# Kernel tuning notes

Measured on AMD Instinct MI355X. Metric: run time of the kernel, lower is better.

## Reference

```python
import jax, jax.numpy as jnp
import numpy as np

B, L, D = 4, 2048, 512
H, DK, DV = 8, 64, 64


def setup_inputs() -> dict:
    key = jax.random.key(0)
    ks = jax.random.split(key, 12)
    s = 0.02
    return {
        "query": jax.random.normal(ks[0], (B, L, D), jnp.float32),
        "key": jax.random.normal(ks[1], (B, L, D), jnp.float32),
        "value": jax.random.normal(ks[2], (B, L, D), jnp.float32),
        "attention_mask": jax.random.normal(ks[3], (1, 1, L, L), jnp.float32),
        "Wq": jax.random.normal(ks[4], (D, H * DK), jnp.float32) * s,
        "bq": jnp.zeros((H * DK,), jnp.float32),
        "Wk": jax.random.normal(ks[5], (D, H * DK), jnp.float32) * s,
        "bk": jnp.zeros((H * DK,), jnp.float32),
        "Wv": jax.random.normal(ks[6], (D, H * DV), jnp.float32) * s,
        "bv": jnp.zeros((H * DV,), jnp.float32),
        "Wo": jax.random.normal(ks[7], (H * DV, D), jnp.float32) * s,
        "bo": jnp.zeros((D,), jnp.float32),
    }


def reference(query, key, value, attention_mask, Wq, bq, Wk, bk, Wv, bv, Wo, bo):
    sz_b, len_q, _ = query.shape
    len_k = key.shape[1]
    # projections -> [B, L, H, d]
    q = (query @ Wq + bq).reshape(sz_b, len_q, H, DK)
    k = (key @ Wk + bk).reshape(sz_b, len_k, H, DK)
    v = (value @ Wv + bv).reshape(sz_b, len_k, H, DV)
    # permute(2,0,1,3): heads first -> [H, B, L, d]
    q = jnp.transpose(q, (2, 0, 1, 3))
    k = jnp.transpose(k, (2, 0, 1, 3))
    v = jnp.transpose(v, (2, 0, 1, 3))
    scale = 1.0 / jnp.sqrt(jnp.asarray(DK, q.dtype))
    scores = jnp.einsum('hbqd,hbkd->hbqk', q, k) * scale + attention_mask
    attn = jax.nn.softmax(scores, axis=-1)
    x = jnp.einsum('hbqk,hbkd->hbqd', attn, v)  # [H, B, Lq, Dv]
    # faithful to torch: transpose(1,2) -> [H, Lq, B, Dv] then view(B, Lq, H*Dv)
    x = jnp.transpose(x, (0, 2, 1, 3)).reshape(sz_b, len_q, H * DV)
    return x @ Wo + bo
```

## Files before the change

kernel.cpp:

```cpp
#include <hip/hip_runtime.h>

#define SEQ    2048
#define DMODEL 512
#define NHEAD  8
#define HDIM   64
#define BATCH  4
#define NROWS  65536
#define KSPLIT 2

#define LOG2E  1.4426950408889634f
#define QSCALE 0.18033688011112042f

typedef float f32x4  __attribute__((ext_vector_type(4)));
typedef float f32x16 __attribute__((ext_vector_type(16)));
typedef _Float16 h16x8 __attribute__((ext_vector_type(8)));
typedef _Float16 h16x2 __attribute__((ext_vector_type(2)));
typedef unsigned int u32x2 __attribute__((ext_vector_type(2)));

union U4H { uint4 u; h16x8 h; };
union U1H2 { unsigned int u; h16x2 h; };

static __device__ inline h16x2 pkrtz(float a, float b) {
    return __builtin_bit_cast(h16x2, __builtin_amdgcn_cvt_pkrtz(a, b));
}
static __device__ inline unsigned short f2h(float x) {
    _Float16 h = (_Float16)x;
    return __builtin_bit_cast(unsigned short, h);
}
static __device__ inline void async_cp16(const void* g, void* l) {
    __builtin_amdgcn_global_load_lds(
        (const __attribute__((address_space(1))) unsigned int*)g,
        (__attribute__((address_space(3))) unsigned int*)l,
        16, 0, 0);
}

struct PrepArgs {
    const float *Wq, *Wk, *Wv, *Wo;
    unsigned short *WqT, *WkT, *WvT, *WoT;
    const float *mask; unsigned short *mp;
    const float *aq, *ak, *av;
    unsigned short *dq, *dk, *dv;
};

__global__ __launch_bounds__(256) void prepass(PrepArgs a) {
    const int bid = blockIdx.x;
    const int t = threadIdx.x;

    if (bid < 1024) {
        const int z = bid >> 8, y = (bid >> 4) & 15, x = bid & 15;
        const float* S; unsigned short* D;
        switch (z) {
            case 0: S = a.Wq; D = a.WqT; break;
            case 1: S = a.Wk; D = a.WkT; break;
            case 2: S = a.Wv; D = a.WvT; break;
            default: S = a.Wo; D = a.WoT; break;
        }
        __shared__ float T[32][33];
        const int r = t >> 3, c = (t & 7) * 4;
        const int k0 = x * 32, n0 = y * 32;
        float4 v = *(const float4*)&S[(size_t)(k0 + r) * DMODEL + n0 + c];
        T[r][c] = v.x; T[r][c + 1] = v.y; T[r][c + 2] = v.z; T[r][c + 3] = v.w;
        __syncthreads();
        ushort4 o;
        o.x = f2h(T[c + 0][r]); o.y = f2h(T[c + 1][r]);
        o.z = f2h(T[c + 2][r]); o.w = f2h(T[c + 3][r]);
        *(ushort4*)&D[(size_t)(n0 + r) * DMODEL + k0 + c] = o;
    } else if (bid < 1024 + 4096) {
        int i = (bid - 1024) * 256 + t;
        int k = (i * 4) & (SEQ - 1);
        int q = (i * 4) >> 11;
        float4 v = ((const float4*)a.mask)[i];
        int kt = k >> 6, kl = k & 63;
        int mt = kl >> 5, g = (kl >> 3) & 3, hl = (kl >> 2) & 1;
        size_t base = ((size_t)kt * SEQ + q) * 64 + hl * 32 + mt * 16 + g * 4;
        ushort4 o;
        o.x = f2h(__builtin_amdgcn_exp2f(v.x * LOG2E));
        o.y = f2h(__builtin_amdgcn_exp2f(v.y * LOG2E));
        o.z = f2h(__builtin_amdgcn_exp2f(v.z * LOG2E));
        o.w = f2h(__builtin_amdgcn_exp2f(v.w * LOG2E));
        *(ushort4*)&a.mp[base] = o;
    } else {
        int u = bid - 5120;
        int z = u >> 11, blk = u & 2047;
        const float* S; unsigned short* D;
        switch (z) {
            case 0: S = a.aq; D = a.dq; break;
            case 1: S = a.ak; D = a.dk; break;
            default: S = a.av; D = a.dv; break;
        }
        size_t i = ((size_t)blk * 256 + t) * 8;
        float4 x = *(const float4*)&S[i];
        float4 y = *(const float4*)&S[i + 4];
        U1H2 p0, p1, p2, p3;
        p0.h = pkrtz(x.x, x.y); p1.h = pkrtz(x.z, x.w);
        p2.h = pkrtz(y.x, y.y); p3.h = pkrtz(y.z, y.w);
        *(uint4*)&D[i] = make_uint4(p0.u, p1.u, p2.u, p3.u);
    }
}

template <int EPI>
static __device__ inline void gemm_core16(
    const unsigned short* __restrict__ Ab, const unsigned short* __restrict__ Bt,
    const float* __restrict__ bias, void* __restrict__ Cout, float oscale,
    int bm, int bn)
{
    __shared__ __align__(16) unsigned short As[2][128 * 32];
    __shared__ __align__(16) unsigned short Bs[2][128 * 32];

    const int t = threadIdx.x;
    const int lane = t & 63, w = t >> 6;
    const int wm = w >> 1, wn = w & 1;
    const int c = lane & 15, quad = lane >> 4;
    const int srow = lane >> 2;
    const int sck  = (lane & 3) ^ ((lane >> 3) & 3);

    f32x4 acc[4][4] = {};

    #pragma unroll
    for (int i = 0; i < 2; i++) {
        int row = 32 * w + 16 * i + srow;
        async_cp16(Ab + (size_t)(bm + row) * DMODEL + sck * 8,
                   &As[0][(32 * w + 16 * i) * 32]);
        async_cp16(Bt + (size_t)(bn + row) * DMODEL + sck * 8,
                   &Bs[0][(32 * w + 16 * i) * 32]);
    }
    __syncthreads();

    const int slot8 = (quad ^ ((c >> 1) & 3)) * 8;

    for (int k0 = 0; k0 < DMODEL; k0 += 32) {
        const int cur = (k0 >> 5) & 1;
        if (k0 + 32 < DMODEL) {
            #pragma unroll
            for (int i = 0; i < 2; i++) {
                int row = 32 * w + 16 * i + srow;
                async_cp16(Ab + (size_t)(bm + row) * DMODEL + k0 + 32 + sck * 8,
                           &As[cur ^ 1][(32 * w + 16 * i) * 32]);
                async_cp16(Bt + (size_t)(bn + row) * DMODEL + k0 + 32 + sck * 8,
                           &Bs[cur ^ 1][(32 * w + 16 * i) * 32]);
            }
        }
        U4H af[4], bf[4];
        #pragma unroll
        for (int mt = 0; mt < 4; mt++)
            af[mt].u = *(const uint4*)&As[cur][(wm * 64 + mt * 16 + c) * 32 + slot8];
        #pragma unroll
        for (int nt = 0; nt < 4; nt++)
            bf[nt].u = *(const uint4*)&Bs[cur][(wn * 64 + nt * 16 + c) * 32 + slot8];
        #pragma unroll
        for (int mt = 0; mt < 4; mt++)
            #pragma unroll
            for (int nt = 0; nt < 4; nt++)
                acc[mt][nt] = __builtin_amdgcn_mfma_f32_16x16x32_f16(
                    af[mt].h, bf[nt].h, acc[mt][nt], 0, 0, 0);
        __syncthreads();
    }

    if (EPI == 2) {
        #pragma unroll
        for (int nt = 0; nt < 4; nt++) {
            int ng = bn + wn * 64 + nt * 16 + c;
            int h = ng >> 6, dv = ng & 63;
            float bv = bias[ng];
            #pragma unroll
            for (int mt = 0; mt < 4; mt++) {
                int mg0 = bm + wm * 64 + mt * 16 + quad * 4;
                int bb = mg0 >> 11, key0 = mg0 & (SEQ - 1);
                U1H2 lo, hi;
                lo.h = pkrtz(acc[mt][nt][0] + bv, acc[mt][nt][1] + bv);
                hi.h = pkrtz(acc[mt][nt][2] + bv, acc[mt][nt][3] + bv);
                *(uint2*)&((unsigned short*)Cout)[
                    ((size_t)(bb * NHEAD + h) * HDIM + dv) * SEQ + key0] =
                    make_uint2(lo.u, hi.u);
            }
        }
        return;
    }
    #pragma unroll
    for (int nt = 0; nt < 4; nt++) {
        int ng = bn + wn * 64 + nt * 16 + c;
        float bv = bias[ng];
        #pragma unroll
        for (int mt = 0; mt < 4; mt++) {
            #pragma unroll
            for (int r = 0; r < 4; r++) {
                int mg = bm + wm * 64 + mt * 16 + quad * 4 + r;
                float v = (acc[mt][nt][r] + bv) * oscale;
                if (EPI == 1)
                    ((unsigned short*)Cout)[(size_t)mg * DMODEL + ng] = f2h(v);
                else
                    ((float*)Cout)[(size_t)mg * DMODEL + ng] = v;
            }
        }
    }
}

struct QKVArgs {
    const unsigned short *A0, *A1, *A2;
    const unsigned short *W0, *W1, *W2;
    const float *b0, *b1, *b2;
    unsigned short *o0, *o1, *o2;
};

__global__ __launch_bounds__(256) void gemm_qkv(QKVArgs a) {
    if (blockIdx.z == 2)
        gemm_core16<2>(a.A2, a.W2, a.b2, a.o2, 1.0f, blockIdx.y * 128, blockIdx.x * 128);
    else if (blockIdx.z == 1)
        gemm_core16<1>(a.A1, a.W1, a.b1, a.o1, 1.0f, blockIdx.y * 128, blockIdx.x * 128);
    else
        gemm_core16<1>(a.A0, a.W0, a.b0, a.o0, QSCALE, blockIdx.y * 128, blockIdx.x * 128);
}

__global__ __launch_bounds__(256) void gemm_fin(
    const unsigned short* __restrict__ A, const unsigned short* __restrict__ W,
    const float* __restrict__ bias, float* __restrict__ C) {
    gemm_core16<0>(A, W, bias, C, 1.0f, blockIdx.y * 128, blockIdx.x * 128);
}

__global__ __launch_bounds__(256, 3) void attn5(
    const unsigned short* __restrict__ qb, const unsigned short* __restrict__ kb,
    const unsigned short* __restrict__ vT, const unsigned short* __restrict__ emp,
    unsigned short* __restrict__ Xp, float* __restrict__ Lp)
{
    __shared__ __align__(16) unsigned short Ks[2][64 * 64];
    __shared__ __align__(16) unsigned short Vs[2][64 * 64];

    const int t = threadIdx.x;
    const int lane = t & 63, w = t >> 6;
    const int c32 = lane & 31, hl = lane >> 5;

    const int bid = blockIdx.x;
    const int xcd = bid & 7, slot = bid >> 3;
    const int bh = slot & 31;
    const int comb = (slot >> 5) * 8 + xcd;
    const int split = comb >> 4;
    const int q0 = (comb & 15) * 128;
    const int b = bh >> 3, head = bh & 7;
    const int qg = q0 + w * 32 + c32;

    const unsigned short* qrow = qb + ((size_t)b * SEQ + qg) * DMODEL + head * HDIM;
    U4H Qf[4];
    #pragma unroll
    for (int s = 0; s < 4; s++)
        Qf[s].u = *(const uint4*)&qrow[s * 16 + hl * 8];

    const unsigned short* kgb = kb + (size_t)b * SEQ * DMODEL + head * HDIM
                              + (size_t)split * 1024 * DMODEL;
    const unsigned short* vgb = vT + (size_t)bh * HDIM * SEQ + split * 1024;

    const int srow = lane >> 3;
    const int sch  = (lane & 7) ^ srow;

    {
        #pragma unroll
        for (int i = 0; i < 2; i++) {
            int row = w * 16 + i * 8 + srow;
            async_cp16(&kgb[(size_t)row * DMODEL + sch * 8], &Ks[0][(w * 16 + i * 8) * 64]);
            async_cp16(&vgb[(size_t)row * SEQ + sch * 8],    &Vs[0][(w * 16 + i * 8) * 64]);
        }
    }

    U4H e0, e1, e2, e3;
    {
        const unsigned short* mrow = emp + ((size_t)(split * 16) * SEQ + qg) * 64 + hl * 32;
        e0.u = *(const uint4*)&mrow[0];
        e1.u = *(const uint4*)&mrow[8];
        e2.u = *(const uint4*)&mrow[16];
        e3.u = *(const uint4*)&mrow[24];
    }

    f32x16 O0 = {}, O1 = {};
    float lsum = 0.f;
    const h16x2 one2 = {(_Float16)1.0f, (_Float16)1.0f};

    for (int kt = 0; kt < 1024 / 64; kt++) {
        const int p = kt & 1;
        __syncthreads();

        if (kt + 1 < 1024 / 64) {
            int k0n = (kt + 1) * 64;
            #pragma unroll
            for (int i = 0; i < 2; i++) {
                int row = w * 16 + i * 8 + srow;
                async_cp16(&kgb[(size_t)(k0n + row) * DMODEL + sch * 8],
                           &Ks[p ^ 1][(w * 16 + i * 8) * 64]);
                async_cp16(&vgb[(size_t)row * SEQ + k0n + sch * 8],
                           &Vs[p ^ 1][(w * 16 + i * 8) * 64]);
            }
        }

        U4H f0, f1, f2, f3;
        {
            int ktn = (kt + 1 < 1024 / 64) ? kt + 1 : kt;
            const unsigned short* mrow =
                emp + ((size_t)(split * 16 + ktn) * SEQ + qg) * 64 + hl * 32;
            f0.u = *(const uint4*)&mrow[0];
            f1.u = *(const uint4*)&mrow[8];
            f2.u = *(const uint4*)&mrow[16];
            f3.u = *(const uint4*)&mrow[24];
        }

        const unsigned short* Kp = Ks[p];
        const unsigned short* Vp = Vs[p];

        f32x16 S0 = {}, S1 = {};
        __builtin_amdgcn_s_setprio(1);
        #pragma unroll
        for (int s = 0; s < 4; s++) {
            int fc = 2 * s + hl;
            int sl = (fc ^ (c32 & 7)) * 8;
            U4H ka0, ka1;
            ka0.u = *(const uint4*)&Kp[c32 * 64 + sl];
            ka1.u = *(const uint4*)&Kp[(32 + c32) * 64 + sl];
            S0 = __builtin_amdgcn_mfma_f32_32x32x16_f16(ka0.h, Qf[s].h, S0, 0, 0, 0);
            S1 = __builtin_amdgcn_mfma_f32_32x32x16_f16(ka1.h, Qf[s].h, S1, 0, 0, 0);
        }
        __builtin_amdgcn_s_setprio(0);

        unsigned int Pf[4][4];
        #pragma unroll
        for (int mt = 0; mt < 2; mt++) {
            f32x16 S = mt ? S1 : S0;
            h16x8 ea = (mt ? e2 : e0).h;
            h16x8 eb = (mt ? e3 : e1).h;
            unsigned int u[4][2];
            #pragma unroll
            for (int jj = 0; jj < 8; jj++) {
                _Float16 exl = (jj < 4) ? ea[2 * jj]     : eb[2 * jj - 8];
                _Float16 exh = (jj < 4) ? ea[2 * jj + 1] : eb[2 * jj - 7];
                h16x2 ex = {exl, exh};
                h16x2 pk = pkrtz(__builtin_amdgcn_exp2f(S[2 * jj]),
                                 __builtin_amdgcn_exp2f(S[2 * jj + 1]));
                h16x2 pp = pk * ex;
#if __has_builtin(__builtin_amdgcn_fdot2)
                lsum = __builtin_amdgcn_fdot2(pp, one2, lsum, false);
#else
                lsum += (float)pp[0] + (float)pp[1];
#endif
                u[jj >> 1][jj & 1] = __builtin_bit_cast(unsigned int, pp);
            }
#if __has_builtin(__builtin_amdgcn_permlane32_swap)
            u32x2 rA0 = __builtin_amdgcn_permlane32_swap(u[0][0], u[1][0], false, false);
            u32x2 rA1 = __builtin_amdgcn_permlane32_swap(u[0][1], u[1][1], false, false);
            u32x2 rB0 = __builtin_amdgcn_permlane32_swap(u[2][0], u[3][0], false, false);
            u32x2 rB1 = __builtin_amdgcn_permlane32_swap(u[2][1], u[3][1], false, false);
            Pf[2 * mt + 0][0] = rA0[0]; Pf[2 * mt + 0][1] = rA1[0];
            Pf[2 * mt + 0][2] = rA0[1]; Pf[2 * mt + 0][3] = rA1[1];
            Pf[2 * mt + 1][0] = rB0[0]; Pf[2 * mt + 1][1] = rB1[0];
            Pf[2 * mt + 1][2] = rB0[1]; Pf[2 * mt + 1][3] = rB1[1];
#else
            unsigned int sA0 = hl ? u[0][0] : u[1][0];
            unsigned int sA1 = hl ? u[0][1] : u[1][1];
            unsigned int sB0 = hl ? u[2][0] : u[3][0];
            unsigned int sB1 = hl ? u[2][1] : u[3][1];
            unsigned int rA0 = (unsigned)__shfl_xor((int)sA0, 32, 64);
            unsigned int rA1 = (unsigned)__shfl_xor((int)sA1, 32, 64);
            unsigned int rB0 = (unsigned)__shfl_xor((int)sB0, 32, 64);
            unsigned int rB1 = (unsigned)__shfl_xor((int)sB1, 32, 64);
            Pf[2 * mt + 0][0] = hl ? rA0 : u[0][0];
            Pf[2 * mt + 0][1] = hl ? rA1 : u[0][1];
            Pf[2 * mt + 0][2] = hl ? u[1][0] : rA0;
            Pf[2 * mt + 0][3] = hl ? u[1][1] : rA1;
            Pf[2 * mt + 1][0] = hl ? rB0 : u[2][0];
            Pf[2 * mt + 1][1] = hl ? rB1 : u[2][1];
            Pf[2 * mt + 1][2] = hl ? u[3][0] : rB0;
            Pf[2 * mt + 1][3] = hl ? u[3][1] : rB1;
#endif
        }

        __builtin_amdgcn_s_setprio(1);
        #pragma unroll
        for (int s = 0; s < 4; s++) {
            int kc = 2 * s + hl;
            int sl = (kc ^ (c32 & 7)) * 8;
            U4H va0, va1, pu;
            va0.u = *(const uint4*)&Vp[c32 * 64 + sl];
            va1.u = *(const uint4*)&Vp[(32 + c32) * 64 + sl];
            pu.u = make_uint4(Pf[s][0], Pf[s][1], Pf[s][2], Pf[s][3]);
            O0 = __builtin_amdgcn_mfma_f32_32x32x16_f16(va0.h, pu.h, O0, 0, 0, 0);
            O1 = __builtin_amdgcn_mfma_f32_32x32x16_f16(va1.h, pu.h, O1, 0, 0, 0);
        }
        __builtin_amdgcn_s_setprio(0);

        e0 = f0; e1 = f1; e2 = f2; e3 = f3;
    }

    lsum += __shfl_xor(lsum, 32, 64);
    const size_t j = ((size_t)head * SEQ + qg) * BATCH + b;
    unsigned short* xr = Xp + ((size_t)split * NROWS + j) * HDIM;
    #pragma unroll
    for (int mt = 0; mt < 2; mt++) {
        f32x16 Ov = mt ? O1 : O0;
        #pragma unroll
        for (int g = 0; g < 4; g++) {
            U1H2 lo, hi;
            lo.h = pkrtz(Ov[g * 4 + 0], Ov[g * 4 + 1]);
            hi.h = pkrtz(Ov[g * 4 + 2], Ov[g * 4 + 3]);
            uint2 st = make_uint2(lo.u, hi.u);
            *(uint2*)&xr[mt * 32 + 8 * g + 4 * hl] = st;
        }
    }
    if (hl == 0) Lp[split * NROWS + j] = lsum;
}

__global__ __launch_bounds__(256) void combine_attn(
    const unsigned short* __restrict__ Xp, const float* __restrict__ Lp,
    unsigned short* __restrict__ xb)
{
    int i = blockIdx.x * 256 + threadIdx.x;
    int j = i >> 3, dc = (i & 7) * 8;
    U4H a, b;
    a.u = *(const uint4*)&Xp[(size_t)j * HDIM + dc];
    b.u = *(const uint4*)&Xp[((size_t)NROWS + j) * HDIM + dc];
    float inv = 1.0f / (Lp[j] + Lp[NROWS + j]);
    U4H o;
    #pragma unroll
    for (int p = 0; p < 4; p++) {
        float s0 = ((float)a.h[2 * p]     + (float)b.h[2 * p])     * inv;
        float s1 = ((float)a.h[2 * p + 1] + (float)b.h[2 * p + 1]) * inv;
        h16x2 pk = pkrtz(s0, s1);
        o.h[2 * p] = pk[0]; o.h[2 * p + 1] = pk[1];
    }
    *(uint4*)&xb[(size_t)j * HDIM + dc] = o.u;
}

extern "C" void kernel_launch(void* const* d_in, const int* in_sizes, int n_in,
                              void* d_out, int out_size, void* d_ws, size_t ws_size,
                              hipStream_t stream) {
    const float* query = (const float*)d_in[0];
    const float* key_  = (const float*)d_in[1];
    const float* value = (const float*)d_in[2];
    const float* mask  = (const float*)d_in[3];
    const float* Wq = (const float*)d_in[4];
    const float* bq = (const float*)d_in[5];
    const float* Wk = (const float*)d_in[6];
    const float* bk = (const float*)d_in[7];
    const float* Wv = (const float*)d_in[8];
    const float* bv = (const float*)d_in[9];
    const float* Wo = (const float*)d_in[10];
    const float* bo = (const float*)d_in[11];
    float* out = (float*)d_out;

    const size_t NP = (size_t)BATCH * SEQ * DMODEL;
    unsigned short* ws   = (unsigned short*)d_ws;
    unsigned short* qb16 = ws;
    unsigned short* kb16 = qb16 + NP;
    unsigned short* vT16 = kb16 + NP;
    unsigned short* xb16 = vT16 + NP;
    unsigned short* em16 = xb16 + NP;
    unsigned short* Xp16 = em16 + (size_t)SEQ * SEQ;
    unsigned short* WqT  = Xp16 + (size_t)KSPLIT * NROWS * HDIM;
    unsigned short* WkT  = WqT + DMODEL * DMODEL;
    unsigned short* WvT  = WkT + DMODEL * DMODEL;
    unsigned short* WoT  = WvT + DMODEL * DMODEL;
    float* Lp = (float*)(WoT + DMODEL * DMODEL);

    unsigned short* q16 = xb16;
    unsigned short* k16 = Xp16;
    unsigned short* v16 = Xp16 + NP;

    PrepArgs pa;
    pa.Wq = Wq; pa.Wk = Wk; pa.Wv = Wv; pa.Wo = Wo;
    pa.WqT = WqT; pa.WkT = WkT; pa.WvT = WvT; pa.WoT = WoT;
    pa.mask = mask; pa.mp = em16;
    pa.aq = query; pa.ak = key_; pa.av = value;
    pa.dq = q16; pa.dk = k16; pa.dv = v16;
    prepass<<<dim3(1024 + 4096 + 6144), 256, 0, stream>>>(pa);

    QKVArgs qa;
    qa.A0 = q16;  qa.A1 = k16;  qa.A2 = v16;
    qa.W0 = WqT;  qa.W1 = WkT;  qa.W2 = WvT;
    qa.b0 = bq;   qa.b1 = bk;   qa.b2 = bv;
    qa.o0 = qb16; qa.o1 = kb16; qa.o2 = vT16;
    gemm_qkv<<<dim3(DMODEL / 128, BATCH * SEQ / 128, 3), 256, 0, stream>>>(qa);

    attn5<<<dim3(BATCH * NHEAD * (SEQ / 128) * KSPLIT), 256, 0, stream>>>(
        qb16, kb16, vT16, em16, Xp16, Lp);

    combine_attn<<<dim3(NROWS * 8 / 256), 256, 0, stream>>>(Xp16, Lp, xb16);

    gemm_fin<<<dim3(DMODEL / 128, BATCH * SEQ / 128), 256, 0, stream>>>(
        xb16, WoT, bo, out);
}
```

Baseline: 235.8 us.

## Triple-buffer LDS tiles with vmcnt waits in GEMM and attention kernels

Both the projection GEMM core and the attention kernel now keep three LDS stages instead of two, prefetching two tiles ahead. The full __syncthreads is replaced by explicit s_waitcnt vmcnt plus s_barrier, so each wave waits only for the older async loads. The attention grid is also changed from a 1D XCD-swizzled index to a plain 3D grid, which drops the XCD-locality mapping. The extra LDS may reduce occupancy, and the vmcnt counts must stay exactly in step with the in-flight global loads, including the mask loads.

```diff
diff --git a/kernel.cpp b/kernel.cpp
--- a/kernel.cpp
+++ b/kernel.cpp
@@ -19,6 +19,8 @@
 
 union U4H { uint4 u; h16x8 h; };
 union U1H2 { unsigned int u; h16x2 h; };
+
+#define WAITV(N) asm volatile("s_waitcnt vmcnt(" #N ")" ::: "memory")
 
 static __device__ inline h16x2 pkrtz(float a, float b) {
     return __builtin_bit_cast(h16x2, __builtin_amdgcn_cvt_pkrtz(a, b));
@@ -104,8 +106,8 @@
     const float* __restrict__ bias, void* __restrict__ Cout, float oscale,
     int bm, int bn)
 {
-    __shared__ __align__(16) unsigned short As[2][128 * 32];
-    __shared__ __align__(16) unsigned short Bs[2][128 * 32];
+    __shared__ __align__(16) unsigned short As[3][128 * 32];
+    __shared__ __align__(16) unsigned short Bs[3][128 * 32];
 
     const int t = threadIdx.x;
     const int lane = t & 63, w = t >> 6;
@@ -116,28 +118,36 @@
 
     f32x4 acc[4][4] = {};
 
+    const int NT = DMODEL / 32;
+
     #pragma unroll
-    for (int i = 0; i < 2; i++) {
-        int row = 32 * w + 16 * i + srow;
-        async_cp16(Ab + (size_t)(bm + row) * DMODEL + sck * 8,
-                   &As[0][(32 * w + 16 * i) * 32]);
-        async_cp16(Bt + (size_t)(bn + row) * DMODEL + sck * 8,
-                   &Bs[0][(32 * w + 16 * i) * 32]);
-    }
-    __syncthreads();
+    for (int b2 = 0; b2 < 2; b2++) {
+        #pragma unroll
+        for (int i = 0; i < 2; i++) {
+            int row = 32 * w + 16 * i + srow;
+            async_cp16(Ab + (size_t)(bm + row) * DMODEL + b2 * 32 + sck * 8,
+                       &As[b2][(32 * w + 16 * i) * 32]);
+            async_cp16(Bt + (size_t)(bn + row) * DMODEL + b2 * 32 + sck * 8,
+                       &Bs[b2][(32 * w + 16 * i) * 32]);
+        }
+    }
+    WAITV(4);
+    __builtin_amdgcn_s_barrier();
 
     const int slot8 = (quad ^ ((c >> 1) & 3)) * 8;
 
-    for (int k0 = 0; k0 < DMODEL; k0 += 32) {
-        const int cur = (k0 >> 5) & 1;
-        if (k0 + 32 < DMODEL) {
+    int cur = 0;
+    for (int p = 0; p < NT; p++) {
+        if (p + 2 < NT) {
+            int nxt = cur + 2; if (nxt >= 3) nxt -= 3;
+            int kn = (p + 2) * 32;
             #pragma unroll
             for (int i = 0; i < 2; i++) {
                 int row = 32 * w + 16 * i + srow;
-                async_cp16(Ab + (size_t)(bm + row) * DMODEL + k0 + 32 + sck * 8,
-                           &As[cur ^ 1][(32 * w + 16 * i) * 32]);
-                async_cp16(Bt + (size_t)(bn + row) * DMODEL + k0 + 32 + sck * 8,
-                           &Bs[cur ^ 1][(32 * w + 16 * i) * 32]);
+                async_cp16(Ab + (size_t)(bm + row) * DMODEL + kn + sck * 8,
+                           &As[nxt][(32 * w + 16 * i) * 32]);
+                async_cp16(Bt + (size_t)(bn + row) * DMODEL + kn + sck * 8,
+                           &Bs[nxt][(32 * w + 16 * i) * 32]);
             }
         }
         U4H af[4], bf[4];
@@ -153,7 +163,11 @@
             for (int nt = 0; nt < 4; nt++)
                 acc[mt][nt] = __builtin_amdgcn_mfma_f32_16x16x32_f16(
                     af[mt].h, bf[nt].h, acc[mt][nt], 0, 0, 0);
-        __syncthreads();
+        if (p + 1 < NT) {
+            if (p + 2 < NT) { WAITV(4); } else { WAITV(0); }
+            __builtin_amdgcn_s_barrier();
+        }
+        cur = cur + 1; if (cur >= 3) cur -= 3;
     }
 
     if (EPI == 2) {
@@ -222,21 +236,17 @@
     const unsigned short* __restrict__ vT, const unsigned short* __restrict__ emp,
     unsigned short* __restrict__ Xp, float* __restrict__ Lp)
 {
-    __shared__ __align__(16) unsigned short Ks[2][64 * 64];
-    __shared__ __align__(16) unsigned short Vs[2][64 * 64];
+    __shared__ __align__(16) unsigned short Ks[3][64 * 64];
+    __shared__ __align__(16) unsigned short Vs[3][64 * 64];
 
     const int t = threadIdx.x;
     const int lane = t & 63, w = t >> 6;
     const int c32 = lane & 31, hl = lane >> 5;
-
-    const int bid = blockIdx.x;
-    const int xcd = bid & 7, slot = bid >> 3;
-    const int bh = slot & 31;
-    const int comb = (slot >> 5) * 8 + xcd;
-    const int split = comb >> 4;
-    const int q0 = (comb & 15) * 128;
-    const int b = bh >> 3, head = bh & 7;
+    const int bh = blockIdx.x, b = bh >> 3, head = bh & 7;
+    const int q0 = blockIdx.y * 128;
+    const int split = blockIdx.z;
     const int qg = q0 + w * 32 + c32;
+    const int NT = 1024 / 64;
 
     const unsigned short* qrow = qb + ((size_t)b * SEQ + qg) * DMODEL + head * HDIM;
     U4H Qf[4];
@@ -250,15 +260,6 @@
 
     const int srow = lane >> 3;
     const int sch  = (lane & 7) ^ srow;
-
-    {
-        #pragma unroll
-        for (int i = 0; i < 2; i++) {
-            int row = w * 16 + i * 8 + srow;
-            async_cp16(&kgb[(size_t)row * DMODEL + sch * 8], &Ks[0][(w * 16 + i * 8) * 64]);
-            async_cp16(&vgb[(size_t)row * SEQ + sch * 8],    &Vs[0][(w * 16 + i * 8) * 64]);
-        }
-    }
 
     U4H e0, e1, e2, e3;
     {
@@ -269,39 +270,52 @@
         e3.u = *(const uint4*)&mrow[24];
     }
 
+    #pragma unroll
+    for (int b2 = 0; b2 < 2; b2++) {
+        int kq = b2 * 64;
+        #pragma unroll
+        for (int i = 0; i < 2; i++) {
+            int row = w * 16 + i * 8 + srow;
+            async_cp16(&kgb[(size_t)(kq + row) * DMODEL + sch * 8],
+                       &Ks[b2][(w * 16 + i * 8) * 64]);
+            async_cp16(&vgb[(size_t)row * SEQ + kq + sch * 8],
+                       &Vs[b2][(w * 16 + i * 8) * 64]);
+        }
+    }
+    WAITV(4);
+    __builtin_amdgcn_s_barrier();
+
     f32x16 O0 = {}, O1 = {};
     float lsum = 0.f;
     const h16x2 one2 = {(_Float16)1.0f, (_Float16)1.0f};
 
-    for (int kt = 0; kt < 1024 / 64; kt++) {
-        const int p = kt & 1;
-        __syncthreads();
-
-        if (kt + 1 < 1024 / 64) {
-            int k0n = (kt + 1) * 64;
+    int cur = 0;
+    for (int kt = 0; kt < NT; kt++) {
+        U4H f0, f1, f2, f3;
+        if (kt + 1 < NT) {
+            const unsigned short* mrow =
+                emp + ((size_t)(split * 16 + kt + 1) * SEQ + qg) * 64 + hl * 32;
+            f0.u = *(const uint4*)&mrow[0];
+            f1.u = *(const uint4*)&mrow[8];
+            f2.u = *(const uint4*)&mrow[16];
+            f3.u = *(const uint4*)&mrow[24];
+        }
+
+        if (kt + 2 < NT) {
+            int nxt = cur + 2; if (nxt >= 3) nxt -= 3;
+            int k0n = (kt + 2) * 64;
             #pragma unroll
             for (int i = 0; i < 2; i++) {
                 int row = w * 16 + i * 8 + srow;
                 async_cp16(&kgb[(size_t)(k0n + row) * DMODEL + sch * 8],
-                           &Ks[p ^ 1][(w * 16 + i * 8) * 64]);
+                           &Ks[nxt][(w * 16 + i * 8) * 64]);
                 async_cp16(&vgb[(size_t)row * SEQ + k0n + sch * 8],
-                           &Vs[p ^ 1][(w * 16 + i * 8) * 64]);
+                           &Vs[nxt][(w * 16 + i * 8) * 64]);
             }
         }
 
-        U4H f0, f1, f2, f3;
-        {
-            int ktn = (kt + 1 < 1024 / 64) ? kt + 1 : kt;
-            const unsigned short* mrow =
-                emp + ((size_t)(split * 16 + ktn) * SEQ + qg) * 64 + hl * 32;
-            f0.u = *(const uint4*)&mrow[0];
-            f1.u = *(const uint4*)&mrow[8];
-            f2.u = *(const uint4*)&mrow[16];
-            f3.u = *(const uint4*)&mrow[24];
-        }
-
-        const unsigned short* Kp = Ks[p];
-        const unsigned short* Vp = Vs[p];
+        const unsigned short* Kp = Ks[cur];
+        const unsigned short* Vp = Vs[cur];
 
         f32x16 S0 = {}, S1 = {};
         __builtin_amdgcn_s_setprio(1);
@@ -382,7 +396,13 @@
         }
         __builtin_amdgcn_s_setprio(0);
 
-        e0 = f0; e1 = f1; e2 = f2; e3 = f3;
+        if (kt + 1 < NT) { e0 = f0; e1 = f1; e2 = f2; e3 = f3; }
+
+        if (kt + 1 < NT) {
+            if (kt + 2 < NT) { WAITV(8); } else { WAITV(4); }
+            __builtin_amdgcn_s_barrier();
+        }
+        cur = cur + 1; if (cur >= 3) cur -= 3;
     }
 
     lsum += __shfl_xor(lsum, 32, 64);
@@ -474,7 +494,7 @@
     qa.o0 = qb16; qa.o1 = kb16; qa.o2 = vT16;
     gemm_qkv<<<dim3(DMODEL / 128, BATCH * SEQ / 128, 3), 256, 0, stream>>>(qa);
 
-    attn5<<<dim3(BATCH * NHEAD * (SEQ / 128) * KSPLIT), 256, 0, stream>>>(
+    attn5<<<dim3(BATCH * NHEAD, SEQ / 128, KSPLIT), 256, 0, stream>>>(
         qb16, kb16, vT16, em16, Xp16, Lp);
 
     combine_attn<<<dim3(NROWS * 8 / 256), 256, 0, stream>>>(Xp16, Lp, xb16);
```

After: 231.7 us. About the same (-1.7%).
